# Optimization experiments

Measured on AMD Instinct MI355X. Metric: run time of the kernel, lower is better.

## Reference

```python
import jax, jax.numpy as jnp
import numpy as np

NN_SIZE = 16  # nn_size from __init__


def _knn_idx(points_ref, k):
    """Brute-force KNN of points_ref against itself (replaces faiss_knn).
    Returns (B, N, k) neighbor indices, self point excluded."""
    sq = jnp.sum(points_ref * points_ref, axis=-1)  # (B, N)
    # squared pairwise distances (B, N, N)
    d2 = sq[:, :, None] + sq[:, None, :] - 2.0 * jnp.einsum(
        'bnd,bmd->bnm', points_ref, points_ref)
    _, idx = jax.lax.top_k(-d2, k + 1)  # nearest first; idx[...,0] is self
    return idx[:, :, 1:]


def _edge_lengths(pts, knn_idx):
    """Gather neighbor coords and compute edge lengths (B, N, K)."""
    group = jax.vmap(lambda p, i: p[i])(pts, knn_idx)  # (B, N, K, D)
    return jnp.linalg.norm(group - pts[:, :, None, :], axis=-1)


def setup_inputs() -> dict:
    key = jax.random.key(0)
    k1, k2 = jax.random.split(key)
    B, N, D = 4, 8192, 3
    points_ref = jax.random.normal(k1, (B, N, D), dtype=jnp.float32)
    # pred points: perturbed ref so the loss is non-degenerate
    points = points_ref + 0.01 * jax.random.normal(k2, (B, N, D), dtype=jnp.float32)
    return {"points_ref": points_ref, "points": points}


def reference(points_ref, points):
    # faiss KNN is non-differentiable -> stop_gradient on the index search
    knn_idx = _knn_idx(jax.lax.stop_gradient(points_ref), NN_SIZE)  # (B,N,K)
    dist_ref = _edge_lengths(points_ref, knn_idx)  # (B, N, K)
    dist = _edge_lengths(points, knn_idx)          # (B, N, K)
    # metric = torch.nn.L1Loss() (mean reduction)
    return jnp.mean(jnp.abs(dist_ref - dist))
```

## Files before the change

kernel.cpp:

```cpp
#include <hip/hip_runtime.h>
#include <math.h>

#define BATCH 4
#define NPTS  8192
#define KNN   16
#define KK    17
#define NQ    (BATCH*NPTS)
#define JMASK 0x1FFFu
#define EMASK 0xFFFFE000u
#define TOTAL_EDGES (BATCH*NPTS*KNN)

#define GC    32
#define GLO   (-4.5f)
#define GINV  (32.0f/9.0f)
#define NCELL (GC*GC*GC)

#define NSG   512
#define SGS   16

#define QPB   16
#define BLOCK 256
#define GRIDQ (NQ/QPB)
#define WIN   64
#define CAP   18
#define NWAVE (BLOCK/64)

__device__ __forceinline__ int cell_coord(float x) {
    int c = (int)floorf((x - GLO) * GINV);
    return min(GC - 1, max(0, c));
}
__device__ __forceinline__ unsigned spread5(unsigned v) {
    v &= 31u;
    v = (v | (v << 8)) & 0x100Fu;
    v = (v | (v << 4)) & 0x10C3u;
    v = (v | (v << 2)) & 0x1249u;
    return v;
}
__device__ __forceinline__ unsigned morton_id(float x, float y, float z) {
    return spread5((unsigned)cell_coord(x)) | (spread5((unsigned)cell_coord(y)) << 1)
         | (spread5((unsigned)cell_coord(z)) << 2);
}
__device__ __forceinline__ unsigned mkkey(const float4 p, float xi, float yi,
                                          float zi, float sqi, unsigned j) {
    const float e  = fmaf(p.x, xi, fmaf(p.y, yi, p.z * zi)) + p.w;
    const float d2 = e + sqi;
    return (__float_as_uint(d2) & EMASK) | j;
}
__device__ __forceinline__ void ins17(unsigned (&a)[KK], unsigned key) {
    #pragma unroll
    for (int k = KK - 1; k >= 1; --k) a[k] = min(a[k], max(a[k - 1], key));
    a[0] = min(a[0], key);
}
template<int RL>
__device__ __forceinline__ unsigned merge_tau(const unsigned (*s_key)[BLOCK], int t) {
    const int mq = t & (QPB - 1), half = (t >> 4) & 1;
    unsigned m[KK];
    #pragma unroll
    for (int k = 0; k < KK; ++k) m[k] = 0xFFFFFFFFu;
    for (int s = 8 * half; s < 8 * half + 8; ++s) {
        const int col = mq + s * QPB;
        for (int k = 0; k < RL; ++k) {
            const unsigned c = s_key[k][col];
            if (c >= m[KK - 1]) break;
            ins17(m, c);
        }
    }
    unsigned tau = 0;
    #pragma unroll
    for (int k = 0; k < KK; ++k) {
        const unsigned bk = (unsigned)__shfl_xor((int)m[KK - 1 - k], 16, 64);
        tau = max(tau, min(m[k], bk));
    }
    return tau;
}

__global__ void pel_hist(const float* __restrict__ pref, unsigned* __restrict__ hist,
                         float* __restrict__ acc, unsigned* __restrict__ bcnt) {
    const int idx = blockIdx.x * 256 + threadIdx.x;
    if (idx == 0) { acc[0] = 0.0f; bcnt[0] = 0u; }
    const int b = idx >> 13;
    const unsigned mid = morton_id(pref[3*idx], pref[3*idx+1], pref[3*idx+2]);
    atomicAdd(&hist[b * NCELL + mid], 1u);
}
__global__ __launch_bounds__(1024)
void pel_scan(const unsigned* __restrict__ hist, unsigned* __restrict__ off) {
    __shared__ unsigned s[1024];
    const unsigned* h = hist + blockIdx.x * NCELL;
    unsigned*       o = off  + blockIdx.x * NCELL;
    const int t = threadIdx.x;
    unsigned v[32], tot = 0;
    #pragma unroll
    for (int k = 0; k < 32; ++k) { v[k] = h[t * 32 + k]; tot += v[k]; }
    s[t] = tot;
    __syncthreads();
    for (int d = 1; d < 1024; d <<= 1) {
        const unsigned add = (t >= d) ? s[t - d] : 0u;
        __syncthreads();
        s[t] += add;
        __syncthreads();
    }
    unsigned run = s[t] - tot;
    #pragma unroll
    for (int k = 0; k < 32; ++k) { o[t * 32 + k] = run; run += v[k]; }
}
__global__ void pel_scatter(const float* __restrict__ pref, const float* __restrict__ pts,
                            unsigned* __restrict__ off,
                            float4* __restrict__ p4r, float4* __restrict__ p4p) {
    const int idx = blockIdx.x * 256 + threadIdx.x;
    const int b = idx >> 13;
    const float x = pref[3*idx], y = pref[3*idx+1], z = pref[3*idx+2];
    const unsigned mid = morton_id(x, y, z);
    const unsigned pos = atomicAdd(&off[b * NCELL + mid], 1u);
    p4r[b * NPTS + pos] = make_float4(-2.f*x, -2.f*y, -2.f*z, fmaf(x, x, fmaf(y, y, z*z)));
    const float px = pts[3*idx], py = pts[3*idx+1], pz = pts[3*idx+2];
    p4p[b * NPTS + pos] = make_float4(-2.f*px, -2.f*py, -2.f*pz,
                                      fmaf(px, px, fmaf(py, py, pz*pz)));
}
__global__ __launch_bounds__(256)
void pel_gstat(const float4* __restrict__ P4r, float4* __restrict__ sgball) {
    const int quad = threadIdx.x >> 4, pos = threadIdx.x & 15;
    const int gid = blockIdx.x * 16 + quad;
    const int b = gid >> 9, s = gid & (NSG - 1);
    const float4 p = P4r[b * NPTS + s * SGS + pos];
    const float x = -0.5f * p.x, y = -0.5f * p.y, z = -0.5f * p.z;
    float mnx = x, mxx = x, mny = y, mxy = y, mnz = z, mxz = z;
    #pragma unroll
    for (int m = 1; m <= 8; m <<= 1) {
        mnx = fminf(mnx, __shfl_xor(mnx, m, 64)); mxx = fmaxf(mxx, __shfl_xor(mxx, m, 64));
        mny = fminf(mny, __shfl_xor(mny, m, 64)); mxy = fmaxf(mxy, __shfl_xor(mxy, m, 64));
        mnz = fminf(mnz, __shfl_xor(mnz, m, 64)); mxz = fmaxf(mxz, __shfl_xor(mxz, m, 64));
    }
    const float cx = 0.5f * (mnx + mxx), cy = 0.5f * (mny + mxy), cz = 0.5f * (mnz + mxz);
    float d = sqrtf((x-cx)*(x-cx) + (y-cy)*(y-cy) + (z-cz)*(z-cz));
    #pragma unroll
    for (int m = 1; m <= 8; m <<= 1) d = fmaxf(d, __shfl_xor(d, m, 64));
    if (pos == 0) sgball[gid] = make_float4(cx, cy, cz, d);
}

__global__ __launch_bounds__(BLOCK, 8)
void pel_query(const float4* __restrict__ P4r, const float4* __restrict__ P4p,
               const float4* __restrict__ sgball,
               float* __restrict__ acc_ws, unsigned* __restrict__ bcnt,
               float* __restrict__ out)
{
    __shared__ unsigned s_key[CAP][BLOCK];
    __shared__ unsigned s_tau[QPB];
    __shared__ unsigned short s_glist[NWAVE][NSG];
    __shared__ int s_ng[NWAVE];
    __shared__ float s_part[NWAVE];

    const int t    = threadIdx.x;
    const int sp   = t & 15, lq = t >> 4;
    const int wv   = t >> 6, lane = t & 63;
    const int q    = blockIdx.x * QPB + lq;
    const int b    = q >> 13;
    const int i    = q & (NPTS - 1);
    const int wcol = lq + sp * QPB;

    const float4* __restrict__ Pq = P4r + b * NPTS;
    const float4* __restrict__ Pp = P4p + b * NPTS;
    const float4* __restrict__ Sg = sgball + b * NSG;

    const float4 self = Pq[i];
    const float xi = -0.5f * self.x, yi = -0.5f * self.y, zi = -0.5f * self.z;
    const float sqi = self.w;

    unsigned al[4] = {~0u, ~0u, ~0u, ~0u};
    const int w0 = min(max(i - WIN / 2, 0), NPTS - WIN) + sp * 4;
    {
        float4 cw[4];
        #pragma unroll
        for (int u = 0; u < 4; ++u) cw[u] = Pq[w0 + u];
        #pragma unroll
        for (int u = 0; u < 4; ++u) {
            const unsigned key = mkkey(cw[u], xi, yi, zi, sqi, (unsigned)(w0 + u));
            #pragma unroll
            for (int k = 3; k >= 1; --k) al[k] = min(al[k], max(al[k - 1], key));
            al[0] = min(al[0], key);
        }
    }
    #pragma unroll
    for (int k = 0; k < 4; ++k) s_key[k][wcol] = al[k];
    __syncthreads();
    if (t < 32) {
        const unsigned tau0 = merge_tau<4>(s_key, t);
        if (t < QPB) s_tau[t] = tau0;
    }
    __syncthreads();

    if (lane == 0) s_ng[wv] = 0;
    float mnx = xi, mxx = xi, mny = yi, mxy = yi, mnz = zi, mxz = zi;
    #pragma unroll
    for (int m = 1; m <= 32; m <<= 1) {
        mnx = fminf(mnx, __shfl_xor(mnx, m, 64)); mxx = fmaxf(mxx, __shfl_xor(mxx, m, 64));
        mny = fminf(mny, __shfl_xor(mny, m, 64)); mxy = fmaxf(mxy, __shfl_xor(mxy, m, 64));
        mnz = fminf(mnz, __shfl_xor(mnz, m, 64)); mxz = fmaxf(mxz, __shfl_xor(mxz, m, 64));
    }
    const float cx = 0.5f * (mnx + mxx), cy = 0.5f * (mny + mxy), cz = 0.5f * (mnz + mxz);
    const float rt = sqrtf(__uint_as_float((s_tau[lq] & EMASK) + 0x2000u));
    float v = sqrtf((xi-cx)*(xi-cx) + (yi-cy)*(yi-cy) + (zi-cz)*(zi-cz)) + rt;
    #pragma unroll
    for (int m = 1; m <= 32; m <<= 1) v = fmaxf(v, __shfl_xor(v, m, 64));
    const float Rq = v + 1e-3f;

    for (int k2 = lane; k2 < NSG; k2 += 64) {
        const float4 gb = Sg[k2];
        const float dx = gb.x - cx, dy = gb.y - cy, dz = gb.z - cz;
        const float rhs = Rq + gb.w;
        if (dx*dx + dy*dy + dz*dz <= rhs * rhs) {
            const int slot = atomicAdd(&s_ng[wv], 1);
            s_glist[wv][slot] = (unsigned short)k2;
        }
    }
    __syncthreads();
    const int ngw = s_ng[wv];

    const unsigned short* __restrict__ gl = s_glist[wv];
    unsigned tauL = s_tau[lq];
    int cnt = 0;
    int j0 = (int)gl[0] * SGS + sp;
    int j1 = (int)gl[min(1, ngw - 1)] * SGS + sp;
    float4 c0 = Pq[j0], c1 = Pq[j1];
    for (int gi = 0; gi < ngw; ++gi) {
        const int jn = (int)gl[min(gi + 2, ngw - 1)] * SGS + sp;
        const float4 nx = Pq[jn];
        const unsigned key = mkkey(c0, xi, yi, zi, sqi, (unsigned)j0);
        s_key[cnt][t] = key;
        cnt += (key <= tauL) ? 1 : 0;
        if (cnt == CAP) {
            unsigned k17[KK];
            #pragma unroll
            for (int k = 0; k < KK; ++k) k17[k] = 0xFFFFFFFFu;
            for (int n = 0; n < cnt; ++n) ins17(k17, s_key[n][t]);
            const unsigned th = k17[KK - 1];
            int kept = 0;
            for (int n = 0; n < cnt; ++n) {
                const unsigned c2 = s_key[n][t];
                if (c2 <= th) { s_key[kept][t] = c2; ++kept; }
            }
            cnt = kept; tauL = min(tauL, th);
        }
        c0 = c1; j0 = j1; c1 = nx; j1 = jn;
    }

    unsigned c17[KK];
    #pragma unroll
    for (int k = 0; k < KK; ++k) c17[k] = 0xFFFFFFFFu;
    for (int n = 0; n < cnt; ++n) ins17(c17, s_key[n][t]);
    __syncthreads();
    #pragma unroll
    for (int k = 0; k < KK; ++k) s_key[k][wcol] = c17[k];
    __syncthreads();
    if (t < 32) {
        const unsigned tauX = merge_tau<KK>(s_key, t);
        if (t < QPB) s_tau[t] = tauX;
    }
    __syncthreads();
    const unsigned tauK = s_tau[lq];

    const float4 selfp = Pp[i];
    const float pxi = -0.5f * selfp.x, pyi = -0.5f * selfp.y, pzi = -0.5f * selfp.z;
    float accv = 0.0f;
    #pragma unroll
    for (int k = 0; k < KK; ++k) {
        if (c17[k] <= tauK) {
            const int j = (int)(c17[k] & JMASK);
            const float4 pr = Pq[j];
            const float er  = fmaf(pr.x, xi, fmaf(pr.y, yi, pr.z * zi)) + pr.w;
            const float d2r = fmaxf(er + sqi, 0.0f);
            const float4 pp = Pp[j];
            const float ep  = fmaf(pp.x, pxi, fmaf(pp.y, pyi, pp.z * pzi)) + pp.w;
            const float d2p = fmaxf(ep + selfp.w, 0.0f);
            accv += fabsf(sqrtf(d2r) - sqrtf(d2p));
        }
    }

    #pragma unroll
    for (int o = 32; o > 0; o >>= 1) accv += __shfl_down(accv, o, 64);
    if (lane == 0) s_part[wv] = accv;
    __syncthreads();
    if (t == 0) {
        float s = 0.0f;
        #pragma unroll
        for (int w2 = 0; w2 < NWAVE; ++w2) s += s_part[w2];
        atomicAdd(acc_ws, s);
        __threadfence();
        const unsigned old = atomicAdd(bcnt, 1u);
        if (old == GRIDQ - 1) {
            __threadfence();
            const float total = atomicAdd(acc_ws, 0.0f);
            out[0] = total * (1.0f / (float)TOTAL_EDGES);
        }
    }
}

extern "C" void kernel_launch(void* const* d_in, const int* in_sizes, int n_in,
                              void* d_out, int out_size, void* d_ws, size_t ws_size,
                              hipStream_t stream) {
    const float* pref = (const float*)d_in[0];
    const float* pts  = (const float*)d_in[1];
    float4*   P4r  = (float4*)d_ws;
    float4*   P4p  = P4r + NQ;
    unsigned* hist = (unsigned*)d_ws;
    unsigned* off  = (unsigned*)((char*)d_ws + 1048576);
    float4*   sgball = (float4*)((char*)d_ws + 1048576);
    float*    acc  = (float*)((char*)d_ws + 1581056);
    unsigned* bcnt = (unsigned*)(acc + 1);
    float*    out  = (float*)d_out;

    hipMemsetAsync(hist, 0, BATCH * NCELL * sizeof(unsigned), stream);
    pel_hist   <<<NQ / 256, 256, 0, stream>>>(pref, hist, acc, bcnt);
    pel_scan   <<<BATCH, 1024, 0, stream>>>(hist, off);
    pel_scatter<<<NQ / 256, 256, 0, stream>>>(pref, pts, off, P4r, P4p);
    pel_gstat  <<<(BATCH * NSG) / 16, 256, 0, stream>>>(P4r, sgball);
    pel_query  <<<GRIDQ, BLOCK, 0, stream>>>(P4r, P4p, sgball, acc, bcnt, out);
}
```

Before: 285.0 us.

## Remap KNN query to one wave with eight lanes per query and register top-k

Rewrites the query kernel to use single-wave blocks handling eight queries, each served by eight lanes scanning two points per neighbor subgroup. The shared-memory candidate buffers and block-level merges are replaced by in-register insertion with a shrinking threshold, shuffle-based bound estimation and a shuffle tournament to find the 17th key. Subgroup list compaction uses ballot/popcount instead of shared atomics. It removes block syncs and LDS traffic but increases per-lane serial work and global atomic count.

```diff
diff --git a/kernel.cpp b/kernel.cpp
--- a/kernel.cpp
+++ b/kernel.cpp
@@ -18,12 +18,9 @@
 #define NSG   512
 #define SGS   16
 
-#define QPB   16
-#define BLOCK 256
-#define GRIDQ (NQ/QPB)
+#define QPW   8
+#define GRIDQ (NQ/QPW)
 #define WIN   64
-#define CAP   18
-#define NWAVE (BLOCK/64)
 
 __device__ __forceinline__ int cell_coord(float x) {
     int c = (int)floorf((x - GLO) * GINV);
@@ -50,28 +47,6 @@
     #pragma unroll
     for (int k = KK - 1; k >= 1; --k) a[k] = min(a[k], max(a[k - 1], key));
     a[0] = min(a[0], key);
-}
-template<int RL>
-__device__ __forceinline__ unsigned merge_tau(const unsigned (*s_key)[BLOCK], int t) {
-    const int mq = t & (QPB - 1), half = (t >> 4) & 1;
-    unsigned m[KK];
-    #pragma unroll
-    for (int k = 0; k < KK; ++k) m[k] = 0xFFFFFFFFu;
-    for (int s = 8 * half; s < 8 * half + 8; ++s) {
-        const int col = mq + s * QPB;
-        for (int k = 0; k < RL; ++k) {
-            const unsigned c = s_key[k][col];
-            if (c >= m[KK - 1]) break;
-            ins17(m, c);
-        }
-    }
-    unsigned tau = 0;
-    #pragma unroll
-    for (int k = 0; k < KK; ++k) {
-        const unsigned bk = (unsigned)__shfl_xor((int)m[KK - 1 - k], 16, 64);
-        tau = max(tau, min(m[k], bk));
-    }
-    return tau;
 }
 
 __global__ void pel_hist(const float* __restrict__ pref, unsigned* __restrict__ hist,
@@ -137,25 +112,19 @@
     if (pos == 0) sgball[gid] = make_float4(cx, cy, cz, d);
 }
 
-__global__ __launch_bounds__(BLOCK, 8)
+__global__ __launch_bounds__(64, 4)
 void pel_query(const float4* __restrict__ P4r, const float4* __restrict__ P4p,
                const float4* __restrict__ sgball,
                float* __restrict__ acc_ws, unsigned* __restrict__ bcnt,
                float* __restrict__ out)
 {
-    __shared__ unsigned s_key[CAP][BLOCK];
-    __shared__ unsigned s_tau[QPB];
-    __shared__ unsigned short s_glist[NWAVE][NSG];
-    __shared__ int s_ng[NWAVE];
-    __shared__ float s_part[NWAVE];
-
-    const int t    = threadIdx.x;
-    const int sp   = t & 15, lq = t >> 4;
-    const int wv   = t >> 6, lane = t & 63;
-    const int q    = blockIdx.x * QPB + lq;
-    const int b    = q >> 13;
-    const int i    = q & (NPTS - 1);
-    const int wcol = lq + sp * QPB;
+    __shared__ unsigned short s_list[NSG];
+
+    const int lane = threadIdx.x;
+    const int lq = lane >> 3, sp = lane & 7;
+    const int q  = blockIdx.x * QPW + lq;
+    const int b  = q >> 13;
+    const int i  = q & (NPTS - 1);
 
     const float4* __restrict__ Pq = P4r + b * NPTS;
     const float4* __restrict__ Pp = P4p + b * NPTS;
@@ -165,30 +134,31 @@
     const float xi = -0.5f * self.x, yi = -0.5f * self.y, zi = -0.5f * self.z;
     const float sqi = self.w;
 
-    unsigned al[4] = {~0u, ~0u, ~0u, ~0u};
-    const int w0 = min(max(i - WIN / 2, 0), NPTS - WIN) + sp * 4;
+    unsigned a3[3] = {~0u, ~0u, ~0u};
+    const int wln = min(max(i - WIN / 2, 0), NPTS - WIN) + sp * 8;
+    #pragma unroll
+    for (int u = 0; u < 8; ++u) {
+        const unsigned key = mkkey(Pq[wln + u], xi, yi, zi, sqi, (unsigned)(wln + u));
+        a3[2] = min(a3[2], max(a3[1], key));
+        a3[1] = min(a3[1], max(a3[0], key));
+        a3[0] = min(a3[0], key);
+    }
+    unsigned tb;
     {
-        float4 cw[4];
-        #pragma unroll
-        for (int u = 0; u < 4; ++u) cw[u] = Pq[w0 + u];
-        #pragma unroll
-        for (int u = 0; u < 4; ++u) {
-            const unsigned key = mkkey(cw[u], xi, yi, zi, sqi, (unsigned)(w0 + u));
-            #pragma unroll
-            for (int k = 3; k >= 1; --k) al[k] = min(al[k], max(al[k - 1], key));
-            al[0] = min(al[0], key);
-        }
-    }
-    #pragma unroll
-    for (int k = 0; k < 4; ++k) s_key[k][wcol] = al[k];
-    __syncthreads();
-    if (t < 32) {
-        const unsigned tau0 = merge_tau<4>(s_key, t);
-        if (t < QPB) s_tau[t] = tau0;
-    }
-    __syncthreads();
-
-    if (lane == 0) s_ng[wv] = 0;
+        const unsigned v0  = a3[2];
+        const unsigned v1  = (unsigned)__shfl_xor((int)v0, 1, 64);
+        const unsigned A   = max(v0, v1), B = min(v0, v1);
+        const unsigned A2  = (unsigned)__shfl_xor((int)A, 2, 64);
+        const unsigned B2  = (unsigned)__shfl_xor((int)B, 2, 64);
+        const unsigned S   = max(A, A2);
+        const unsigned U   = max(min(A, A2), max(B, B2));
+        const unsigned S4  = (unsigned)__shfl_xor((int)S, 4, 64);
+        const unsigned U4  = (unsigned)__shfl_xor((int)U, 4, 64);
+        tb = max(min(S, S4), max(U, U4));
+    }
+    const unsigned bound = tb;
+    const float rt = sqrtf(__uint_as_float((bound & EMASK) + 0x2000u));
+
     float mnx = xi, mxx = xi, mny = yi, mxy = yi, mnz = zi, mxz = zi;
     #pragma unroll
     for (int m = 1; m <= 32; m <<= 1) {
@@ -196,67 +166,62 @@
         mny = fminf(mny, __shfl_xor(mny, m, 64)); mxy = fmaxf(mxy, __shfl_xor(mxy, m, 64));
         mnz = fminf(mnz, __shfl_xor(mnz, m, 64)); mxz = fmaxf(mxz, __shfl_xor(mxz, m, 64));
     }
-    const float cx = 0.5f * (mnx + mxx), cy = 0.5f * (mny + mxy), cz = 0.5f * (mnz + mxz);
-    const float rt = sqrtf(__uint_as_float((s_tau[lq] & EMASK) + 0x2000u));
-    float v = sqrtf((xi-cx)*(xi-cx) + (yi-cy)*(yi-cy) + (zi-cz)*(zi-cz)) + rt;
+    const float cxw = 0.5f * (mnx + mxx), cyw = 0.5f * (mny + mxy), czw = 0.5f * (mnz + mxz);
+    float v = sqrtf((xi-cxw)*(xi-cxw) + (yi-cyw)*(yi-cyw) + (zi-czw)*(zi-czw)) + rt;
     #pragma unroll
     for (int m = 1; m <= 32; m <<= 1) v = fmaxf(v, __shfl_xor(v, m, 64));
     const float Rq = v + 1e-3f;
 
-    for (int k2 = lane; k2 < NSG; k2 += 64) {
+    int ng = 0;
+    #pragma unroll
+    for (int r = 0; r < NSG / 64; ++r) {
+        const int k2 = r * 64 + lane;
         const float4 gb = Sg[k2];
-        const float dx = gb.x - cx, dy = gb.y - cy, dz = gb.z - cz;
+        const float dx = gb.x - cxw, dy = gb.y - cyw, dz = gb.z - czw;
         const float rhs = Rq + gb.w;
-        if (dx*dx + dy*dy + dz*dz <= rhs * rhs) {
-            const int slot = atomicAdd(&s_ng[wv], 1);
-            s_glist[wv][slot] = (unsigned short)k2;
-        }
+        const bool acc = (dx*dx + dy*dy + dz*dz <= rhs * rhs);
+        const unsigned long long mask = __ballot(acc);
+        if (acc)
+            s_list[ng + (int)__popcll(mask & ((1ull << lane) - 1ull))] = (unsigned short)k2;
+        ng += (int)__popcll(mask);
     }
     __syncthreads();
-    const int ngw = s_ng[wv];
-
-    const unsigned short* __restrict__ gl = s_glist[wv];
-    unsigned tauL = s_tau[lq];
-    int cnt = 0;
-    int j0 = (int)gl[0] * SGS + sp;
-    int j1 = (int)gl[min(1, ngw - 1)] * SGS + sp;
-    float4 c0 = Pq[j0], c1 = Pq[j1];
-    for (int gi = 0; gi < ngw; ++gi) {
-        const int jn = (int)gl[min(gi + 2, ngw - 1)] * SGS + sp;
-        const float4 nx = Pq[jn];
-        const unsigned key = mkkey(c0, xi, yi, zi, sqi, (unsigned)j0);
-        s_key[cnt][t] = key;
-        cnt += (key <= tauL) ? 1 : 0;
-        if (cnt == CAP) {
-            unsigned k17[KK];
-            #pragma unroll
-            for (int k = 0; k < KK; ++k) k17[k] = 0xFFFFFFFFu;
-            for (int n = 0; n < cnt; ++n) ins17(k17, s_key[n][t]);
-            const unsigned th = k17[KK - 1];
-            int kept = 0;
-            for (int n = 0; n < cnt; ++n) {
-                const unsigned c2 = s_key[n][t];
-                if (c2 <= th) { s_key[kept][t] = c2; ++kept; }
-            }
-            cnt = kept; tauL = min(tauL, th);
-        }
-        c0 = c1; j0 = j1; c1 = nx; j1 = jn;
-    }
 
     unsigned c17[KK];
     #pragma unroll
     for (int k = 0; k < KK; ++k) c17[k] = 0xFFFFFFFFu;
-    for (int n = 0; n < cnt; ++n) ins17(c17, s_key[n][t]);
-    __syncthreads();
-    #pragma unroll
-    for (int k = 0; k < KK; ++k) s_key[k][wcol] = c17[k];
-    __syncthreads();
-    if (t < 32) {
-        const unsigned tauX = merge_tau<KK>(s_key, t);
-        if (t < QPB) s_tau[t] = tauX;
-    }
-    __syncthreads();
-    const unsigned tauK = s_tau[lq];
+    unsigned tauL = bound;
+    const int sp2 = sp * 2;
+    int j0 = (int)s_list[0] * SGS + sp2;
+    int j1 = (int)s_list[min(1, ng - 1)] * SGS + sp2;
+    float4 c0a = Pq[j0], c0b = Pq[j0 + 1];
+    float4 c1a = Pq[j1], c1b = Pq[j1 + 1];
+    for (int e = 0; e < ng; ++e) {
+        const int jn = (int)s_list[min(e + 2, ng - 1)] * SGS + sp2;
+        const float4 nxa = Pq[jn], nxb = Pq[jn + 1];
+        unsigned key = mkkey(c0a, xi, yi, zi, sqi, (unsigned)j0);
+        if (key <= tauL) { ins17(c17, key); tauL = min(tauL, c17[KK - 1]); }
+        key = mkkey(c0b, xi, yi, zi, sqi, (unsigned)(j0 + 1));
+        if (key <= tauL) { ins17(c17, key); tauL = min(tauL, c17[KK - 1]); }
+        c0a = c1a; c0b = c1b; j0 = j1;
+        c1a = nxa; c1b = nxb; j1 = jn;
+    }
+
+    unsigned cpy[KK];
+    #pragma unroll
+    for (int k = 0; k < KK; ++k) cpy[k] = c17[k];
+    unsigned tauK = 0xFFFFFFFFu;
+    for (int r = 0; r < KK; ++r) {
+        const unsigned h  = cpy[0];
+        unsigned m1 = min(h,  (unsigned)__shfl_xor((int)h,  1, 64));
+        m1          = min(m1, (unsigned)__shfl_xor((int)m1, 2, 64));
+        const unsigned w = min(m1, (unsigned)__shfl_xor((int)m1, 4, 64));
+        const bool won = (h == w);
+        #pragma unroll
+        for (int k = 0; k < KK - 1; ++k) cpy[k] = won ? cpy[k + 1] : cpy[k];
+        cpy[KK - 1] = won ? 0xFFFFFFFFu : cpy[KK - 1];
+        tauK = w;
+    }
 
     const float4 selfp = Pp[i];
     const float pxi = -0.5f * selfp.x, pyi = -0.5f * selfp.y, pzi = -0.5f * selfp.z;
@@ -277,13 +242,8 @@
 
     #pragma unroll
     for (int o = 32; o > 0; o >>= 1) accv += __shfl_down(accv, o, 64);
-    if (lane == 0) s_part[wv] = accv;
-    __syncthreads();
-    if (t == 0) {
-        float s = 0.0f;
-        #pragma unroll
-        for (int w2 = 0; w2 < NWAVE; ++w2) s += s_part[w2];
-        atomicAdd(acc_ws, s);
+    if (lane == 0) {
+        atomicAdd(acc_ws, accv);
         __threadfence();
         const unsigned old = atomicAdd(bcnt, 1u);
         if (old == GRIDQ - 1) {
@@ -313,5 +273,5 @@
     pel_scan   <<<BATCH, 1024, 0, stream>>>(hist, off);
     pel_scatter<<<NQ / 256, 256, 0, stream>>>(pref, pts, off, P4r, P4p);
     pel_gstat  <<<(BATCH * NSG) / 16, 256, 0, stream>>>(P4r, sgball);
-    pel_query  <<<GRIDQ, BLOCK, 0, stream>>>(P4r, P4p, sgball, acc, bcnt, out);
-}
+    pel_query  <<<GRIDQ, 64, 0, stream>>>(P4r, P4p, sgball, acc, bcnt, out);
+}
```

After: 309.5 us. +8.6%, slower.
